# Kernel tuning notes

Measured on AMD Instinct MI355X. Metric: run time of the kernel, lower is better.

Reference implementation:

```python
import jax, jax.numpy as jnp
import numpy as np

B, C, L = 32, 8, 2048
K, S = 512, 64  # num_shapelets, shapelets_size


def setup_inputs() -> dict:
    key = jax.random.key(0)
    k1, k2 = jax.random.split(key)
    x = jax.random.normal(k1, (B, C, L), dtype=jnp.float32)
    shapelets = jax.random.normal(k2, (C, K, S), dtype=jnp.float32)
    return {"x": x, "shapelets": shapelets}


def reference(x, shapelets):
    # x: [B, C, L]; shapelets: [C, K, S]
    s = shapelets.shape[-1]
    n_dims = x.shape[1]
    W = x.shape[2] - s + 1  # number of sliding windows
    # unfold(2, S, 1): gather overlapping windows -> [B, C, W, S]
    idx = jnp.arange(W)[:, None] + jnp.arange(s)[None, :]
    xw = x[:, :, idx]
    # L2-normalize windows along window length (clamp min like torch)
    xw = xw / jnp.maximum(jnp.linalg.norm(xw, axis=-1, keepdims=True), 1e-8)
    # L2-normalize shapelets along length
    sn = shapelets / jnp.maximum(jnp.linalg.norm(shapelets, axis=-1, keepdims=True), 1e-8)
    # matmul [B,C,W,S] @ [C,S,K] then sum over C, fused into one einsum -> [B, W, K]
    sim = jnp.einsum('bcws,cks->bwk', xw, sn) / n_dims
    sim = jax.nn.relu(sim)
    # max over window positions -> [B, K]; keep the singleton channel dim like torch ([B,1,K])
    out = jnp.max(sim, axis=1)
    return out[:, None, :]
```

## Files before the change

kernel.cpp:

```cpp
#include <hip/hip_runtime.h>


#define B_ 32
#define C_ 8
#define L_ 2048
#define K_ 512
#define S_ 64
#define W_ 1985
#define XS_ 2176

typedef _Float16 f16x8  __attribute__((ext_vector_type(8)));
typedef _Float16 f16x8u __attribute__((ext_vector_type(8), aligned(4)));
typedef float    f32x16 __attribute__((ext_vector_type(16)));

__global__ __launch_bounds__(256)
void prep_k(const float* __restrict__ x, const float* __restrict__ sh,
            _Float16* __restrict__ Bp, float* __restrict__ invn,
            _Float16* __restrict__ xh0, _Float16* __restrict__ xh1,
            float* __restrict__ out) {
    __shared__ float xr[L_];
    const int tid = threadIdx.x;
    const int blk = blockIdx.x;

    if (blk < 128) {
        const int sb   = blk * 4 + (tid >> 6);
        const int c    = sb >> 6;
        const int kq   = (sb >> 4) & 3;
        const int nt   = sb & 15;
        const int lane = tid & 63;
        const int half = lane >> 5;
        const int q    = nt * 32 + (lane & 31);

        const float4* sp = (const float4*)(sh + (size_t)(c * K_ + q) * S_);
        float ss = 0.f;
        #pragma unroll
        for (int i = 0; i < 8; ++i) {
            float4 v = sp[half * 8 + i];
            ss += v.x * v.x + v.y * v.y + v.z * v.z + v.w * v.w;
        }
        ss += __shfl_xor(ss, 32);
        float inv = 1.f / fmaxf(sqrtf(ss), 1e-8f);

        float4 u0 = sp[kq * 4 + half * 2];
        float4 u1 = sp[kq * 4 + half * 2 + 1];
        f16x8 o;
        o[0] = (_Float16)(u0.x * inv); o[1] = (_Float16)(u0.y * inv);
        o[2] = (_Float16)(u0.z * inv); o[3] = (_Float16)(u0.w * inv);
        o[4] = (_Float16)(u1.x * inv); o[5] = (_Float16)(u1.y * inv);
        o[6] = (_Float16)(u1.z * inv); o[7] = (_Float16)(u1.w * inv);
        ((f16x8*)Bp)[((c * 4 + kq) * 16 + nt) * 64 + lane] = o;
    } else {
        const int r = blk - 128;
        const float* xp = x + (size_t)r * L_;
        for (int i = tid; i < L_ / 4; i += 256)
            ((float4*)xr)[i] = ((const float4*)xp)[i];
        __syncthreads();

        float* ivp = invn + (size_t)r * L_;
        const int w0 = tid * 8;
        float ss = 0.f;
        if (w0 < W_) {
            #pragma unroll
            for (int j = 0; j < S_; ++j) { float v = xr[w0 + j]; ss += v * v; }
        }
        #pragma unroll
        for (int u = 0; u < 8; ++u) {
            int w = w0 + u;
            float o = 0.f;
            if (u > 0 && w < W_)
                ss += xr[w + 63] * xr[w + 63] - xr[w - 1] * xr[w - 1];
            if (w < W_) o = 0.125f / fmaxf(sqrtf(ss), 1e-8f);
            if (w < L_) ivp[w] = o;
        }

        _Float16* p0 = xh0 + (size_t)r * XS_;
        _Float16* p1 = xh1 + (size_t)r * XS_;
        for (int i = tid; i < XS_ / 8; i += 256) {
            f16x8 o0, o1;
            #pragma unroll
            for (int j = 0; j < 8; ++j) {
                int e = i * 8 + j;
                o0[j] = (_Float16)((e     < L_) ? xr[e]     : 0.f);
                o1[j] = (_Float16)((e + 1 < L_) ? xr[e + 1] : 0.f);
            }
            ((f16x8*)p0)[i] = o0;
            ((f16x8*)p1)[i] = o1;
        }
        if (r < 64) out[r * 256 + tid] = 0.f;
    }
}

__device__ __forceinline__ void glds16(const void* g, void* l) {
    __builtin_amdgcn_global_load_lds(
        (const __attribute__((address_space(1))) unsigned int*)g,
        (__attribute__((address_space(3))) unsigned int*)l, 16, 0, 0);
}

__device__ __forceinline__ void loadA(
    int c, const _Float16* __restrict__ xbase, const float* __restrict__ ivbase,
    int m0, int m1, f16x8 (&ar)[8], float (&iv)[2])
{
    iv[0] = ivbase[(size_t)c * L_ + m0];
    iv[1] = ivbase[(size_t)c * L_ + m1];
    const _Float16* xp = xbase + (size_t)c * XS_;
    #pragma unroll
    for (int mt = 0; mt < 2; ++mt)
        #pragma unroll
        for (int ks = 0; ks < 4; ++ks)
            ar[mt * 4 + ks] = *(const f16x8u*)(xp + mt * 32 + ks * 16);
}

__device__ __forceinline__ void compC(
    int c, const f16x8* __restrict__ bsl, int lane,
    const f16x8 (&ar)[8], const float (&iv)[2], f32x16 (&acc)[2][2])
{
    f16x8 bf[8];
    #pragma unroll
    for (int ks = 0; ks < 4; ++ks)
        #pragma unroll
        for (int nt = 0; nt < 2; ++nt)
            bf[ks * 2 + nt] = bsl[(c * 8 + ks * 2 + nt) * 64 + lane];

    const _Float16 h0 = (_Float16)iv[0], h1 = (_Float16)iv[1];
    f16x8 is0, is1;
    #pragma unroll
    for (int j = 0; j < 8; ++j) { is0[j] = h0; is1[j] = h1; }

    __builtin_amdgcn_s_setprio(1);
    #pragma unroll
    for (int ks = 0; ks < 4; ++ks) {
        f16x8 a0 = ar[0 * 4 + ks] * is0;
        f16x8 a1 = ar[1 * 4 + ks] * is1;
        #pragma unroll
        for (int nt = 0; nt < 2; ++nt) {
            acc[0][nt] = __builtin_amdgcn_mfma_f32_32x32x16_f16(
                a0, bf[ks * 2 + nt], acc[0][nt], 0, 0, 0);
            acc[1][nt] = __builtin_amdgcn_mfma_f32_32x32x16_f16(
                a1, bf[ks * 2 + nt], acc[1][nt], 0, 0, 0);
        }
    }
    __builtin_amdgcn_s_setprio(0);
}

__global__ __launch_bounds__(256, 2)
void mcs_k(const _Float16* __restrict__ xh0, const _Float16* __restrict__ xh1,
           const _Float16* __restrict__ Bp, const float* __restrict__ invn,
           float* __restrict__ out) {
    const int wt  = blockIdx.x;
    const int ng  = blockIdx.y;
    const int b   = blockIdx.z;
    const int tid = threadIdx.x;
    const int lane = tid & 63;
    const int wv   = tid >> 6;

    const int l31 = lane & 31;
    const int lh  = lane >> 5;
    const int Wb  = wt * 256 + wv * 64;
    const int m0  = Wb + l31;
    const int m1  = Wb + 32 + l31;

    __shared__ f16x8 Bs[64][64];

    {
        const f16x8* bp = (const f16x8*)Bp;
        #pragma unroll
        for (int u = 0; u < 16; ++u) {
            const int e   = wv * 16 + u;
            const int c   = e >> 3;
            const int sub = e & 7;
            const int src = ((c * 4 + (sub >> 1)) * 16 + ng * 2 + (sub & 1)) * 64;
            glds16(bp + src + lane, &Bs[e][0]);
        }
    }

    const _Float16* xb = (l31 & 1) ? (xh1 - 1) : xh0;
    const _Float16* xbase = xb + (size_t)b * C_ * XS_ + Wb + l31 + lh * 8;
    const float*   ivbase = invn + (size_t)b * C_ * L_;

    f32x16 acc[2][2];
    #pragma unroll
    for (int mt = 0; mt < 2; ++mt)
        #pragma unroll
        for (int nt = 0; nt < 2; ++nt)
            #pragma unroll
            for (int r = 0; r < 16; ++r) acc[mt][nt][r] = 0.f;

    f16x8 aA[8], aB[8];
    float ivA[2], ivB[2];

    loadA(0, xbase, ivbase, m0, m1, aA, ivA);
    __syncthreads();

    #pragma unroll 1
    for (int cp = 0; cp < 4; ++cp) {
        const int c0 = cp * 2;
        loadA(c0 + 1, xbase, ivbase, m0, m1, aB, ivB);
        compC(c0, &Bs[0][0], lane, aA, ivA, acc);
        if (cp < 3)
            loadA(c0 + 2, xbase, ivbase, m0, m1, aA, ivA);
        compC(c0 + 1, &Bs[0][0], lane, aB, ivB, acc);
    }

    #pragma unroll
    for (int nt = 0; nt < 2; ++nt) {
        float v = 0.f;
        #pragma unroll
        for (int mt = 0; mt < 2; ++mt)
            #pragma unroll
            for (int r = 0; r < 16; ++r) v = fmaxf(v, acc[mt][nt][r]);
        v = fmaxf(v, __shfl_xor(v, 32));
        if (lane < 32)
            atomicMax((unsigned int*)(out + (size_t)b * K_ + ng * 64 + nt * 32 + l31),
                      __float_as_uint(v));
    }
}

extern "C" void kernel_launch(void* const* d_in, const int* in_sizes, int n_in,
                              void* d_out, int out_size, void* d_ws, size_t ws_size,
                              hipStream_t stream) {
    const float* x  = (const float*)d_in[0];
    const float* sh = (const float*)d_in[1];
    float* out = (float*)d_out;

    _Float16* Bp   = (_Float16*)d_ws;
    float*    invn = (float*)((char*)d_ws + (512 << 10));
    _Float16* xh0  = (_Float16*)((char*)d_ws + (512 << 10) + (2 << 20));
    _Float16* xh1  = xh0 + (size_t)B_ * C_ * XS_;

    prep_k<<<dim3(384), dim3(256), 0, stream>>>(x, sh, Bp, invn, xh0, xh1, out);
    mcs_k<<<dim3(8, 8, B_), dim3(256), 0, stream>>>(xh0, xh1, Bp, invn, out);
}
```

Baseline: 98.81 us.

## Split each block's window tile across 8 waves and reduce max in LDS

Each wave now covers 32 windows instead of 64, so the block grows to 512 threads and each wave holds half the accumulators and A fragments. This lowers register pressure and adds waves for latency hiding. Per-wave maxima are combined in shared memory before a single atomicMax per column, which cuts global atomic traffic. The cost is an extra __syncthreads and an LDS reduction, plus the B fragments in LDS are now reused by fewer MFMAs per wave.

```diff
diff --git a/kernel.cpp b/kernel.cpp
--- a/kernel.cpp
+++ b/kernel.cpp
@@ -98,21 +98,18 @@
 
 __device__ __forceinline__ void loadA(
     int c, const _Float16* __restrict__ xbase, const float* __restrict__ ivbase,
-    int m0, int m1, f16x8 (&ar)[8], float (&iv)[2])
+    int m0, f16x8 (&ar)[4], float &iv)
 {
-    iv[0] = ivbase[(size_t)c * L_ + m0];
-    iv[1] = ivbase[(size_t)c * L_ + m1];
+    iv = ivbase[(size_t)c * L_ + m0];
     const _Float16* xp = xbase + (size_t)c * XS_;
     #pragma unroll
-    for (int mt = 0; mt < 2; ++mt)
-        #pragma unroll
-        for (int ks = 0; ks < 4; ++ks)
-            ar[mt * 4 + ks] = *(const f16x8u*)(xp + mt * 32 + ks * 16);
+    for (int ks = 0; ks < 4; ++ks)
+        ar[ks] = *(const f16x8u*)(xp + ks * 16);
 }
 
 __device__ __forceinline__ void compC(
     int c, const f16x8* __restrict__ bsl, int lane,
-    const f16x8 (&ar)[8], const float (&iv)[2], f32x16 (&acc)[2][2])
+    const f16x8 (&ar)[4], float iv, f32x16 (&acc)[2])
 {
     f16x8 bf[8];
     #pragma unroll
@@ -121,28 +118,24 @@
         for (int nt = 0; nt < 2; ++nt)
             bf[ks * 2 + nt] = bsl[(c * 8 + ks * 2 + nt) * 64 + lane];
 
-    const _Float16 h0 = (_Float16)iv[0], h1 = (_Float16)iv[1];
-    f16x8 is0, is1;
-    #pragma unroll
-    for (int j = 0; j < 8; ++j) { is0[j] = h0; is1[j] = h1; }
+    const _Float16 h = (_Float16)iv;
+    f16x8 is;
+    #pragma unroll
+    for (int j = 0; j < 8; ++j) is[j] = h;
 
     __builtin_amdgcn_s_setprio(1);
     #pragma unroll
     for (int ks = 0; ks < 4; ++ks) {
-        f16x8 a0 = ar[0 * 4 + ks] * is0;
-        f16x8 a1 = ar[1 * 4 + ks] * is1;
-        #pragma unroll
-        for (int nt = 0; nt < 2; ++nt) {
-            acc[0][nt] = __builtin_amdgcn_mfma_f32_32x32x16_f16(
-                a0, bf[ks * 2 + nt], acc[0][nt], 0, 0, 0);
-            acc[1][nt] = __builtin_amdgcn_mfma_f32_32x32x16_f16(
-                a1, bf[ks * 2 + nt], acc[1][nt], 0, 0, 0);
-        }
+        f16x8 a = ar[ks] * is;
+        acc[0] = __builtin_amdgcn_mfma_f32_32x32x16_f16(
+            a, bf[ks * 2 + 0], acc[0], 0, 0, 0);
+        acc[1] = __builtin_amdgcn_mfma_f32_32x32x16_f16(
+            a, bf[ks * 2 + 1], acc[1], 0, 0, 0);
     }
     __builtin_amdgcn_s_setprio(0);
 }
 
-__global__ __launch_bounds__(256, 2)
+__global__ __launch_bounds__(512, 4)
 void mcs_k(const _Float16* __restrict__ xh0, const _Float16* __restrict__ xh1,
            const _Float16* __restrict__ Bp, const float* __restrict__ invn,
            float* __restrict__ out) {
@@ -155,17 +148,17 @@
 
     const int l31 = lane & 31;
     const int lh  = lane >> 5;
-    const int Wb  = wt * 256 + wv * 64;
+    const int Wb  = wt * 256 + wv * 32;
     const int m0  = Wb + l31;
-    const int m1  = Wb + 32 + l31;
 
     __shared__ f16x8 Bs[64][64];
+    __shared__ float red[8][2][32];
 
     {
         const f16x8* bp = (const f16x8*)Bp;
         #pragma unroll
-        for (int u = 0; u < 16; ++u) {
-            const int e   = wv * 16 + u;
+        for (int u = 0; u < 8; ++u) {
+            const int e   = wv * 8 + u;
             const int c   = e >> 3;
             const int sub = e & 7;
             const int src = ((c * 4 + (sub >> 1)) * 16 + ng * 2 + (sub & 1)) * 64;
@@ -177,41 +170,50 @@
     const _Float16* xbase = xb + (size_t)b * C_ * XS_ + Wb + l31 + lh * 8;
     const float*   ivbase = invn + (size_t)b * C_ * L_;
 
-    f32x16 acc[2][2];
-    #pragma unroll
-    for (int mt = 0; mt < 2; ++mt)
-        #pragma unroll
-        for (int nt = 0; nt < 2; ++nt)
-            #pragma unroll
-            for (int r = 0; r < 16; ++r) acc[mt][nt][r] = 0.f;
-
-    f16x8 aA[8], aB[8];
-    float ivA[2], ivB[2];
-
-    loadA(0, xbase, ivbase, m0, m1, aA, ivA);
+    f32x16 acc[2];
+    #pragma unroll
+    for (int nt = 0; nt < 2; ++nt)
+        #pragma unroll
+        for (int r = 0; r < 16; ++r) acc[nt][r] = 0.f;
+
+    f16x8 aA[4], aB[4];
+    float ivA, ivB;
+
+    loadA(0, xbase, ivbase, m0, aA, ivA);
     __syncthreads();
 
     #pragma unroll 1
     for (int cp = 0; cp < 4; ++cp) {
         const int c0 = cp * 2;
-        loadA(c0 + 1, xbase, ivbase, m0, m1, aB, ivB);
+        loadA(c0 + 1, xbase, ivbase, m0, aB, ivB);
         compC(c0, &Bs[0][0], lane, aA, ivA, acc);
         if (cp < 3)
-            loadA(c0 + 2, xbase, ivbase, m0, m1, aA, ivA);
+            loadA(c0 + 2, xbase, ivbase, m0, aA, ivA);
         compC(c0 + 1, &Bs[0][0], lane, aB, ivB, acc);
     }
 
+    float m[2];
     #pragma unroll
     for (int nt = 0; nt < 2; ++nt) {
         float v = 0.f;
         #pragma unroll
-        for (int mt = 0; mt < 2; ++mt)
-            #pragma unroll
-            for (int r = 0; r < 16; ++r) v = fmaxf(v, acc[mt][nt][r]);
+        for (int r = 0; r < 16; ++r) v = fmaxf(v, acc[nt][r]);
         v = fmaxf(v, __shfl_xor(v, 32));
-        if (lane < 32)
-            atomicMax((unsigned int*)(out + (size_t)b * K_ + ng * 64 + nt * 32 + l31),
-                      __float_as_uint(v));
+        m[nt] = v;
+    }
+    if (lane < 32) {
+        red[wv][0][l31] = m[0];
+        red[wv][1][l31] = m[1];
+    }
+    __syncthreads();
+    if (tid < 64) {
+        const int nt  = tid >> 5;
+        const int col = tid & 31;
+        float v = red[0][nt][col];
+        #pragma unroll
+        for (int w2 = 1; w2 < 8; ++w2) v = fmaxf(v, red[w2][nt][col]);
+        atomicMax((unsigned int*)(out + (size_t)b * K_ + ng * 64 + nt * 32 + col),
+                  __float_as_uint(v));
     }
 }
 
@@ -228,5 +230,5 @@
     _Float16* xh1  = xh0 + (size_t)B_ * C_ * XS_;
 
     prep_k<<<dim3(384), dim3(256), 0, stream>>>(x, sh, Bp, invn, xh0, xh1, out);
-    mcs_k<<<dim3(8, 8, B_), dim3(256), 0, stream>>>(xh0, xh1, Bp, invn, out);
-}
+    mcs_k<<<dim3(8, 8, B_), dim3(512), 0, stream>>>(xh0, xh1, Bp, invn, out);
+}
```

After: 100.0 us. Within noise of the previous version (+1.2%).

## Stage x window slabs in LDS via async global_load_lds instead of per-lane global loads

Applied to the files above, without the earlier changes.

The GEMM kernel now copies each block's 416-element fp16 slab of both x parity copies for all channels into shared memory, using async global-to-LDS loads issued alongside the B-tile copy. It then builds A fragments from 32-bit LDS reads rather than the unaligned 16-byte global loads used before. This drops the manual two-stage register double buffer in favour of a simple channel loop unrolled by two. The intent is to cut redundant, misaligned global traffic for overlapping windows. In exchange it adds LDS usage and many scalar LDS reads, which may affect occupancy and cause bank conflicts. The workspace layout is also reordered.

```diff
diff --git a/kernel.cpp b/kernel.cpp
--- a/kernel.cpp
+++ b/kernel.cpp
@@ -8,9 +8,10 @@
 #define S_ 64
 #define W_ 1985
 #define XS_ 2176
+#define XSLAB_ 416
+#define XSLDW_ 208
 
 typedef _Float16 f16x8  __attribute__((ext_vector_type(8)));
-typedef _Float16 f16x8u __attribute__((ext_vector_type(8), aligned(4)));
 typedef float    f32x16 __attribute__((ext_vector_type(16)));
 
 __global__ __launch_bounds__(256)
@@ -96,51 +97,7 @@
         (__attribute__((address_space(3))) unsigned int*)l, 16, 0, 0);
 }
 
-__device__ __forceinline__ void loadA(
-    int c, const _Float16* __restrict__ xbase, const float* __restrict__ ivbase,
-    int m0, int m1, f16x8 (&ar)[8], float (&iv)[2])
-{
-    iv[0] = ivbase[(size_t)c * L_ + m0];
-    iv[1] = ivbase[(size_t)c * L_ + m1];
-    const _Float16* xp = xbase + (size_t)c * XS_;
-    #pragma unroll
-    for (int mt = 0; mt < 2; ++mt)
-        #pragma unroll
-        for (int ks = 0; ks < 4; ++ks)
-            ar[mt * 4 + ks] = *(const f16x8u*)(xp + mt * 32 + ks * 16);
-}
-
-__device__ __forceinline__ void compC(
-    int c, const f16x8* __restrict__ bsl, int lane,
-    const f16x8 (&ar)[8], const float (&iv)[2], f32x16 (&acc)[2][2])
-{
-    f16x8 bf[8];
-    #pragma unroll
-    for (int ks = 0; ks < 4; ++ks)
-        #pragma unroll
-        for (int nt = 0; nt < 2; ++nt)
-            bf[ks * 2 + nt] = bsl[(c * 8 + ks * 2 + nt) * 64 + lane];
-
-    const _Float16 h0 = (_Float16)iv[0], h1 = (_Float16)iv[1];
-    f16x8 is0, is1;
-    #pragma unroll
-    for (int j = 0; j < 8; ++j) { is0[j] = h0; is1[j] = h1; }
-
-    __builtin_amdgcn_s_setprio(1);
-    #pragma unroll
-    for (int ks = 0; ks < 4; ++ks) {
-        f16x8 a0 = ar[0 * 4 + ks] * is0;
-        f16x8 a1 = ar[1 * 4 + ks] * is1;
-        #pragma unroll
-        for (int nt = 0; nt < 2; ++nt) {
-            acc[0][nt] = __builtin_amdgcn_mfma_f32_32x32x16_f16(
-                a0, bf[ks * 2 + nt], acc[0][nt], 0, 0, 0);
-            acc[1][nt] = __builtin_amdgcn_mfma_f32_32x32x16_f16(
-                a1, bf[ks * 2 + nt], acc[1][nt], 0, 0, 0);
-        }
-    }
-    __builtin_amdgcn_s_setprio(0);
-}
+union AFrag { unsigned int u[4]; f16x8 v; };
 
 __global__ __launch_bounds__(256, 2)
 void mcs_k(const _Float16* __restrict__ xh0, const _Float16* __restrict__ xh1,
@@ -155,11 +112,13 @@
 
     const int l31 = lane & 31;
     const int lh  = lane >> 5;
-    const int Wb  = wt * 256 + wv * 64;
-    const int m0  = Wb + l31;
-    const int m1  = Wb + 32 + l31;
-
-    __shared__ f16x8 Bs[64][64];
+    const int WBLK = wt * 256;
+    const int Wb   = WBLK + wv * 64;
+    const int m0   = Wb + l31;
+    const int m1   = Wb + 32 + l31;
+
+    __shared__ __attribute__((aligned(16))) f16x8   Bs[64][64];
+    __shared__ __attribute__((aligned(16))) _Float16 xs[16 * XSLAB_];
 
     {
         const f16x8* bp = (const f16x8*)Bp;
@@ -172,10 +131,19 @@
             glds16(bp + src + lane, &Bs[e][0]);
         }
     }
-
-    const _Float16* xb = (l31 & 1) ? (xh1 - 1) : xh0;
-    const _Float16* xbase = xb + (size_t)b * C_ * XS_ + Wb + l31 + lh * 8;
-    const float*   ivbase = invn + (size_t)b * C_ * L_;
+    if (lane < 52) {
+        #pragma unroll
+        for (int u = 0; u < 4; ++u) {
+            const int r   = wv * 4 + u;
+            const int c   = r >> 1;
+            const int par = r & 1;
+            const _Float16* srcp = (par ? xh1 : xh0)
+                + (size_t)(b * C_ + c) * XS_ + WBLK + lane * 8;
+            glds16(srcp, &xs[r * XSLAB_]);
+        }
+    }
+
+    const float* ivbase = invn + (size_t)b * C_ * L_;
 
     f32x16 acc[2][2];
     #pragma unroll
@@ -185,20 +153,50 @@
             #pragma unroll
             for (int r = 0; r < 16; ++r) acc[mt][nt][r] = 0.f;
 
-    f16x8 aA[8], aB[8];
-    float ivA[2], ivB[2];
-
-    loadA(0, xbase, ivbase, m0, m1, aA, ivA);
+    const int par = l31 & 1;
+    const unsigned int* xsl = (const unsigned int*)xs;
+    const int xdw0 = par * XSLDW_ + ((wv * 64 + l31 - par) >> 1) + lh * 4;
+
     __syncthreads();
 
-    #pragma unroll 1
-    for (int cp = 0; cp < 4; ++cp) {
-        const int c0 = cp * 2;
-        loadA(c0 + 1, xbase, ivbase, m0, m1, aB, ivB);
-        compC(c0, &Bs[0][0], lane, aA, ivA, acc);
-        if (cp < 3)
-            loadA(c0 + 2, xbase, ivbase, m0, m1, aA, ivA);
-        compC(c0 + 1, &Bs[0][0], lane, aB, ivB, acc);
+    #pragma unroll 2
+    for (int c = 0; c < C_; ++c) {
+        AFrag g[6];
+        const int cb = c * (2 * XSLDW_) + xdw0;
+        #pragma unroll
+        for (int p = 0; p < 6; ++p)
+            #pragma unroll
+            for (int t = 0; t < 4; ++t)
+                g[p].u[t] = xsl[cb + p * 8 + t];
+
+        const float iv0 = ivbase[(size_t)c * L_ + m0];
+        const float iv1 = ivbase[(size_t)c * L_ + m1];
+        const _Float16 h0 = (_Float16)iv0, h1 = (_Float16)iv1;
+        f16x8 is0, is1;
+        #pragma unroll
+        for (int j = 0; j < 8; ++j) { is0[j] = h0; is1[j] = h1; }
+
+        f16x8 bf[8];
+        #pragma unroll
+        for (int ks = 0; ks < 4; ++ks)
+            #pragma unroll
+            for (int nt = 0; nt < 2; ++nt)
+                bf[ks * 2 + nt] = Bs[c * 8 + ks * 2 + nt][lane];
+
+        __builtin_amdgcn_s_setprio(1);
+        #pragma unroll
+        for (int ks = 0; ks < 4; ++ks) {
+            f16x8 a0 = g[ks].v     * is0;
+            f16x8 a1 = g[ks + 2].v * is1;
+            #pragma unroll
+            for (int nt = 0; nt < 2; ++nt) {
+                acc[0][nt] = __builtin_amdgcn_mfma_f32_32x32x16_f16(
+                    a0, bf[ks * 2 + nt], acc[0][nt], 0, 0, 0);
+                acc[1][nt] = __builtin_amdgcn_mfma_f32_32x32x16_f16(
+                    a1, bf[ks * 2 + nt], acc[1][nt], 0, 0, 0);
+            }
+        }
+        __builtin_amdgcn_s_setprio(0);
     }
 
     #pragma unroll
@@ -223,9 +221,9 @@
     float* out = (float*)d_out;
 
     _Float16* Bp   = (_Float16*)d_ws;
-    float*    invn = (float*)((char*)d_ws + (512 << 10));
-    _Float16* xh0  = (_Float16*)((char*)d_ws + (512 << 10) + (2 << 20));
+    _Float16* xh0  = (_Float16*)((char*)d_ws + (512 << 10));
     _Float16* xh1  = xh0 + (size_t)B_ * C_ * XS_;
+    float*    invn = (float*)(xh1 + (size_t)B_ * C_ * XS_);
 
     prep_k<<<dim3(384), dim3(256), 0, stream>>>(x, sh, Bp, invn, xh0, xh1, out);
     mcs_k<<<dim3(8, 8, B_), dim3(256), 0, stream>>>(xh0, xh1, Bp, invn, out);
```

After: 95.10 us. 3.7% less time.

## Pre-expand x into per-lane MFMA panels for aligned coalesced A loads

Applied to the files above, without the earlier changes.

Replaces the two shifted fp16 copies of x with a panel layout written by the prep kernel, where each lane's 8-element window fragment is stored contiguously. The main kernel then does aligned 16-byte coalesced loads and reuses overlapping panels, needing 6 vector loads per channel instead of 8 unaligned ones. This cuts misaligned global-load overhead at the cost of a larger workspace and more prep-side writes.

```diff
diff --git a/kernel.cpp b/kernel.cpp
--- a/kernel.cpp
+++ b/kernel.cpp
@@ -7,17 +7,15 @@
 #define K_ 512
 #define S_ 64
 #define W_ 1985
-#define XS_ 2176
+#define NP_ 130
 
 typedef _Float16 f16x8  __attribute__((ext_vector_type(8)));
-typedef _Float16 f16x8u __attribute__((ext_vector_type(8), aligned(4)));
 typedef float    f32x16 __attribute__((ext_vector_type(16)));
 
 __global__ __launch_bounds__(256)
 void prep_k(const float* __restrict__ x, const float* __restrict__ sh,
             _Float16* __restrict__ Bp, float* __restrict__ invn,
-            _Float16* __restrict__ xh0, _Float16* __restrict__ xh1,
-            float* __restrict__ out) {
+            _Float16* __restrict__ AX, float* __restrict__ out) {
     __shared__ float xr[L_];
     const int tid = threadIdx.x;
     const int blk = blockIdx.x;
@@ -73,18 +71,20 @@
             if (w < L_) ivp[w] = o;
         }
 
-        _Float16* p0 = xh0 + (size_t)r * XS_;
-        _Float16* p1 = xh1 + (size_t)r * XS_;
-        for (int i = tid; i < XS_ / 8; i += 256) {
-            f16x8 o0, o1;
+        _Float16* axp = AX + (size_t)r * (NP_ * 512);
+        const int lane = tid & 63;
+        const int wvp  = tid >> 6;
+        const int kof  = (lane & 31) + (lane >> 5) * 8;
+        #pragma unroll 1
+        for (int P = wvp; P < NP_; P += 4) {
+            const int base = P * 16 + kof;
+            f16x8 o;
             #pragma unroll
             for (int j = 0; j < 8; ++j) {
-                int e = i * 8 + j;
-                o0[j] = (_Float16)((e     < L_) ? xr[e]     : 0.f);
-                o1[j] = (_Float16)((e + 1 < L_) ? xr[e + 1] : 0.f);
+                int e = base + j;
+                o[j] = (_Float16)xr[e < L_ ? e : L_ - 1];
             }
-            ((f16x8*)p0)[i] = o0;
-            ((f16x8*)p1)[i] = o1;
+            *((f16x8*)(axp + (size_t)P * 512) + lane) = o;
         }
         if (r < 64) out[r * 256 + tid] = 0.f;
     }
@@ -97,29 +97,27 @@
 }
 
 __device__ __forceinline__ void loadA(
-    int c, const _Float16* __restrict__ xbase, const float* __restrict__ ivbase,
-    int m0, int m1, f16x8 (&ar)[8], float (&iv)[2])
+    int c, const f16x8* __restrict__ axl, const float* __restrict__ ivbase,
+    int m0, int m1, f16x8 (&g)[6], float (&iv)[2])
 {
     iv[0] = ivbase[(size_t)c * L_ + m0];
     iv[1] = ivbase[(size_t)c * L_ + m1];
-    const _Float16* xp = xbase + (size_t)c * XS_;
-    #pragma unroll
-    for (int mt = 0; mt < 2; ++mt)
-        #pragma unroll
-        for (int ks = 0; ks < 4; ++ks)
-            ar[mt * 4 + ks] = *(const f16x8u*)(xp + mt * 32 + ks * 16);
+    const f16x8* u = axl + (size_t)c * (NP_ * 64);
+    #pragma unroll
+    for (int p = 0; p < 6; ++p)
+        g[p] = u[p * 64];
 }
 
 __device__ __forceinline__ void compC(
-    int c, const f16x8* __restrict__ bsl, int lane,
-    const f16x8 (&ar)[8], const float (&iv)[2], f32x16 (&acc)[2][2])
+    int c, const f16x8* __restrict__ Bsl, int lane,
+    const f16x8 (&g)[6], const float (&iv)[2], f32x16 (&acc)[2][2])
 {
     f16x8 bf[8];
     #pragma unroll
     for (int ks = 0; ks < 4; ++ks)
         #pragma unroll
         for (int nt = 0; nt < 2; ++nt)
-            bf[ks * 2 + nt] = bsl[(c * 8 + ks * 2 + nt) * 64 + lane];
+            bf[ks * 2 + nt] = Bsl[(c * 8 + ks * 2 + nt) * 64 + lane];
 
     const _Float16 h0 = (_Float16)iv[0], h1 = (_Float16)iv[1];
     f16x8 is0, is1;
@@ -129,8 +127,8 @@
     __builtin_amdgcn_s_setprio(1);
     #pragma unroll
     for (int ks = 0; ks < 4; ++ks) {
-        f16x8 a0 = ar[0 * 4 + ks] * is0;
-        f16x8 a1 = ar[1 * 4 + ks] * is1;
+        f16x8 a0 = g[ks]     * is0;
+        f16x8 a1 = g[ks + 2] * is1;
         #pragma unroll
         for (int nt = 0; nt < 2; ++nt) {
             acc[0][nt] = __builtin_amdgcn_mfma_f32_32x32x16_f16(
@@ -143,9 +141,8 @@
 }
 
 __global__ __launch_bounds__(256, 2)
-void mcs_k(const _Float16* __restrict__ xh0, const _Float16* __restrict__ xh1,
-           const _Float16* __restrict__ Bp, const float* __restrict__ invn,
-           float* __restrict__ out) {
+void mcs_k(const _Float16* __restrict__ AX, const _Float16* __restrict__ Bp,
+           const float* __restrict__ invn, float* __restrict__ out) {
     const int wt  = blockIdx.x;
     const int ng  = blockIdx.y;
     const int b   = blockIdx.z;
@@ -154,12 +151,12 @@
     const int wv   = tid >> 6;
 
     const int l31 = lane & 31;
-    const int lh  = lane >> 5;
     const int Wb  = wt * 256 + wv * 64;
     const int m0  = Wb + l31;
     const int m1  = Wb + 32 + l31;
-
-    __shared__ f16x8 Bs[64][64];
+    const int P0  = wt * 16 + wv * 4;
+
+    __shared__ __attribute__((aligned(16))) f16x8 Bs[64][64];
 
     {
         const f16x8* bp = (const f16x8*)Bp;
@@ -173,9 +170,8 @@
         }
     }
 
-    const _Float16* xb = (l31 & 1) ? (xh1 - 1) : xh0;
-    const _Float16* xbase = xb + (size_t)b * C_ * XS_ + Wb + l31 + lh * 8;
-    const float*   ivbase = invn + (size_t)b * C_ * L_;
+    const f16x8* axl = (const f16x8*)AX + ((size_t)(b * C_) * NP_ + P0) * 64 + lane;
+    const float* ivbase = invn + (size_t)b * C_ * L_;
 
     f32x16 acc[2][2];
     #pragma unroll
@@ -185,20 +181,20 @@
             #pragma unroll
             for (int r = 0; r < 16; ++r) acc[mt][nt][r] = 0.f;
 
-    f16x8 aA[8], aB[8];
+    f16x8 gA[6], gB[6];
     float ivA[2], ivB[2];
 
-    loadA(0, xbase, ivbase, m0, m1, aA, ivA);
+    loadA(0, axl, ivbase, m0, m1, gA, ivA);
     __syncthreads();
 
     #pragma unroll 1
     for (int cp = 0; cp < 4; ++cp) {
         const int c0 = cp * 2;
-        loadA(c0 + 1, xbase, ivbase, m0, m1, aB, ivB);
-        compC(c0, &Bs[0][0], lane, aA, ivA, acc);
+        loadA(c0 + 1, axl, ivbase, m0, m1, gB, ivB);
+        compC(c0, &Bs[0][0], lane, gA, ivA, acc);
         if (cp < 3)
-            loadA(c0 + 2, xbase, ivbase, m0, m1, aA, ivA);
-        compC(c0 + 1, &Bs[0][0], lane, aB, ivB, acc);
+            loadA(c0 + 2, axl, ivbase, m0, m1, gA, ivA);
+        compC(c0 + 1, &Bs[0][0], lane, gB, ivB, acc);
     }
 
     #pragma unroll
@@ -224,9 +220,8 @@
 
     _Float16* Bp   = (_Float16*)d_ws;
     float*    invn = (float*)((char*)d_ws + (512 << 10));
-    _Float16* xh0  = (_Float16*)((char*)d_ws + (512 << 10) + (2 << 20));
-    _Float16* xh1  = xh0 + (size_t)B_ * C_ * XS_;
-
-    prep_k<<<dim3(384), dim3(256), 0, stream>>>(x, sh, Bp, invn, xh0, xh1, out);
-    mcs_k<<<dim3(8, 8, B_), dim3(256), 0, stream>>>(xh0, xh1, Bp, invn, out);
-}
+    _Float16* AX   = (_Float16*)((char*)d_ws + (512 << 10) + (2 << 20));
+
+    prep_k<<<dim3(384), dim3(256), 0, stream>>>(x, sh, Bp, invn, AX, out);
+    mcs_k<<<dim3(8, 8, B_), dim3(256), 0, stream>>>(AX, Bp, invn, out);
+}
```

Result: slower. 106.5 us (+7.7%).
